# Kernel tuning notes

Measured on AMD Instinct MI355X. Metric: run time of the kernel, lower is better.

The kernel has to match this reference:

```python
import jax, jax.numpy as jnp
import numpy as np

N, K, B, D, T = 30000, 32, 8, 256, 10
NC = T + 1            # int_small_classes
LB_COL, UB_COL = 21, 22
INF = 1e18


def _ln(x, g, b, eps=1e-5):
    m = jnp.mean(x, axis=-1, keepdims=True)
    v = jnp.mean((x - m) ** 2, axis=-1, keepdims=True)
    return (x - m) * jax.lax.rsqrt(v + eps) * g + b


def _head(x, ng, nb, W1, b1, W2, b2, Wh, bh):
    # LayerNorm -> Linear -> GELU -> Linear -> GELU -> residual -> head (dropout off: eval)
    h = _ln(x, ng, nb)
    h = jax.nn.gelu(h @ W1.T + b1, approximate=False)
    h = jax.nn.gelu(h @ W2.T + b2, approximate=False)
    return (x + h) @ Wh.T + bh


def setup_inputs():
    key = jax.random.key(0)
    ks = jax.random.split(key, 32)
    s = 0.05
    inp = {}
    inp['evolved_tokens'] = jax.random.normal(ks[0], (B * K, D), jnp.float32)
    inp['var_batch'] = jnp.sort(jax.random.randint(ks[1], (N,), 0, B))
    aw = jax.random.uniform(ks[2], (N, K), jnp.float32)
    inp['attn_weights'] = aw / aw.sum(-1, keepdims=True)
    inp['var_types'] = jax.random.randint(ks[3], (N,), 0, 3)
    inp['z_var_0'] = jax.random.normal(ks[4], (N, D), jnp.float32)
    vf = 0.1 * jax.random.normal(ks[5], (N, 23), jnp.float32)
    lb = jnp.floor(jax.random.uniform(ks[6], (N,), minval=-5.0, maxval=0.0))
    ub = lb + jnp.floor(jax.random.uniform(ks[7], (N,), minval=0.0, maxval=30.0))
    ub = jnp.where(jax.random.uniform(ks[8], (N,)) < 0.1, 1e19, ub)
    inp['variable_features'] = vf.at[:, LB_COL].set(lb).at[:, UB_COL].set(ub)
    # deslice proj + fusion norm
    inp['Wp'] = s * jax.random.normal(ks[9], (D, D), jnp.float32)
    inp['bp'] = jnp.zeros((D,), jnp.float32)
    inp['fn_g'] = jnp.ones((D,), jnp.float32)
    inp['fn_b'] = jnp.zeros((D,), jnp.float32)
    # three decoder heads
    i = 10
    for name, out in (('bin', 1), ('ints', NC), ('intl', 1)):
        inp[name + '_ng'] = jnp.ones((D,), jnp.float32)
        inp[name + '_nb'] = jnp.zeros((D,), jnp.float32)
        inp[name + '_W1'] = s * jax.random.normal(ks[i], (D, D), jnp.float32)
        inp[name + '_b1'] = jnp.zeros((D,), jnp.float32)
        inp[name + '_W2'] = s * jax.random.normal(ks[i + 1], (D, D), jnp.float32)
        inp[name + '_b2'] = jnp.zeros((D,), jnp.float32)
        inp[name + '_Wh'] = s * jax.random.normal(ks[i + 2], (out, D), jnp.float32)
        inp[name + '_bh'] = (jnp.full((out,), -0.5, jnp.float32) if name == 'bin'
                             else jnp.zeros((out,), jnp.float32))
        i += 3
    return inp


def reference(evolved_tokens, var_batch, attn_weights, var_types, z_var_0,
              variable_features, Wp, bp, fn_g, fn_b,
              bin_ng, bin_nb, bin_W1, bin_b1, bin_W2, bin_b2, bin_Wh, bin_bh,
              ints_ng, ints_nb, ints_W1, ints_b1, ints_W2, ints_b2, ints_Wh, ints_bh,
              intl_ng, intl_nb, intl_W1, intl_b1, intl_W2, intl_b2, intl_Wh, intl_bh):
    # 1. deslice: attn_weights @ projected evolved tokens of the variable's graph
    proj = evolved_tokens @ Wp.T + bp          # [B*K, D]
    tok3 = proj.reshape(B, K, D)
    z_des = jnp.einsum('nk,nkd->nd', attn_weights, tok3[var_batch])  # [N, D]
    # 2. residual fusion + LayerNorm
    z_out = _ln(z_des + z_var_0, fn_g, fn_b)
    # 3. routing (extract_int_routing)
    lb = variable_features[:, LB_COL]
    ub = variable_features[:, UB_COL]
    is_int = var_types == 2
    finite = (jnp.abs(lb) < INF) & (jnp.abs(ub) < INF)
    mask_int_small = is_int & finite & ((ub - lb) <= T)
    mask_int_large = is_int & ~mask_int_small
    mask_bin = var_types == 1
    offsets = jnp.floor(lb)                                   # [N]
    ranges = jnp.clip(jnp.ceil(ub) - offsets + 1.0, 1.0, NC).astype(jnp.int32)  # [N]
    # 4. decode. Heads are evaluated densely on all N rows; the original's
    #    gather->MLP->scatter equals row-selection of these dense outputs.
    prob_bin = jax.nn.sigmoid(_head(z_out, bin_ng, bin_nb, bin_W1, bin_b1,
                                    bin_W2, bin_b2, bin_Wh, bin_bh))   # [N, 1]
    logits = _head(z_out, ints_ng, ints_nb, ints_W1, ints_b1,
                   ints_W2, ints_b2, ints_Wh, ints_bh)                 # [N, NC]
    valid = jnp.arange(NC)[None, :] < ranges[:, None]
    logits = jnp.where(valid, logits, -1e9)  # dynamic logit masking of invalid classes
    pred_large = _head(z_out, intl_ng, intl_nb, intl_W1, intl_b1,
                       intl_W2, intl_b2, intl_Wh, intl_bh)             # [N, 1]
    return (z_out, prob_bin, logits, pred_large,
            mask_bin, mask_int_small, mask_int_large, offsets, ranges)
```

## Files before the change

### kernel.cpp

```cpp
#include <hip/hip_runtime.h>
#include <math.h>

#define NV   30000
#define DD   256
#define KK   32
#define NCLS 11
#define NT   469

#define OZ  0
#define OPB 7680000
#define OLG 7710000
#define OPL 8040000
#define OMB 8070000
#define OMS 8100000
#define OML 8130000
#define OOF 8160000
#define ORG 8190000

typedef __bf16 bf16x8 __attribute__((ext_vector_type(8)));
typedef float  f32x4  __attribute__((ext_vector_type(4)));

__device__ __forceinline__ unsigned short f2b(float f) {
    unsigned u = __float_as_uint(f);
    u += 0x7fffu + ((u >> 16) & 1u);
    return (unsigned short)(u >> 16);
}

__device__ __forceinline__ float gelu_f(float x) {
    float x2 = x * x;
    float m = x * __builtin_fmaf(-0.0713548163f, x2, -1.5957691216f);
    float e = __expf(m);
    return x * __builtin_amdgcn_rcpf(1.0f + e);
}

__device__ __forceinline__ int swz(int row) { return (row + (row >> 3)) & 7; }
__device__ __forceinline__ int lidx(int row, int col) {
    return row * 256 + ((((col) >> 3) ^ swz(row)) << 3) + (col & 7);
}

struct WP {
    const float *W1, *ng, *nb, *b1, *W2, *Wh;
    unsigned short *W1e, *W2b, *Whb;
    float *b1e, *swh;
    int nc;
};

__global__ void k_prep(const float* __restrict__ et, const float* __restrict__ Wp,
                       const float* __restrict__ bp, unsigned short* __restrict__ projb,
                       WP wa, WP wb, WP wc) {
    __shared__ float es[DD];
    __shared__ float red[4], red2[4];
    if (blockIdx.y == 0) {
        int r = blockIdx.x, c = threadIdx.x;
        es[c] = et[r * DD + c];
        __syncthreads();
        const float4* w4 = (const float4*)(Wp + c * DD);
        float acc = bp[c];
#pragma unroll 16
        for (int d = 0; d < DD / 4; ++d) {
            float4 w = w4[d];
            acc += es[4 * d] * w.x + es[4 * d + 1] * w.y + es[4 * d + 2] * w.z + es[4 * d + 3] * w.w;
        }
        projb[r * DD + c] = f2b(acc);
        return;
    }
    WP wp = (blockIdx.y == 1) ? wa : ((blockIdx.y == 2) ? wb : wc);
    int j = blockIdx.x, d = threadIdx.x;
    float v1 = wp.W1[j * DD + d];
    wp.W1e[j * DD + d] = f2b(v1 * wp.ng[d]);
    wp.W2b[j * DD + d] = f2b(wp.W2[j * DD + d]);
    float p2 = 0.f;
    if (j < 16) {
        p2 = (j < wp.nc) ? wp.Wh[j * DD + d] : 0.f;
        wp.Whb[j * DD + d] = f2b(p2);
    }
    float p = v1 * wp.nb[d];
#pragma unroll
    for (int m = 1; m < 64; m <<= 1) { p += __shfl_xor(p, m); p2 += __shfl_xor(p2, m); }
    if ((d & 63) == 0) { red[d >> 6] = p; red2[d >> 6] = p2; }
    __syncthreads();
    if (d == 0) {
        wp.b1e[j] = wp.b1[j] + red[0] + red[1] + red[2] + red[3];
        if (j < 16) wp.swh[j] = red2[0] + red2[1] + red2[2] + red2[3];
    }
}

__global__ __launch_bounds__(256)
void k_zout(const unsigned short* __restrict__ projb, const int* __restrict__ vb,
            const float* __restrict__ aw, const float* __restrict__ z0,
            const float* __restrict__ g, const float* __restrict__ b,
            const float* __restrict__ vf, const int* __restrict__ vt,
            float* __restrict__ out, unsigned short* __restrict__ zhat,
            float2* __restrict__ zstat) {
    int wv = threadIdx.x >> 6, lane = threadIdx.x & 63;
    int n = blockIdx.x * 4 + wv;
    if (n >= NV) return;
    int bidx = vb[n];
    float awv = aw[n * KK + (lane & 31)];
    const ushort4* pr = (const ushort4*)(projb + (size_t)bidx * KK * DD);
    float4 acc = ((const float4*)(z0 + (size_t)n * DD))[lane];
#pragma unroll 8
    for (int k = 0; k < KK; ++k) {
        float a = __shfl(awv, k);
        ushort4 pu = pr[k * 64 + lane];
        acc.x += a * __uint_as_float((unsigned)pu.x << 16);
        acc.y += a * __uint_as_float((unsigned)pu.y << 16);
        acc.z += a * __uint_as_float((unsigned)pu.z << 16);
        acc.w += a * __uint_as_float((unsigned)pu.w << 16);
    }
    float s = acc.x + acc.y + acc.z + acc.w;
    float q = acc.x * acc.x + acc.y * acc.y + acc.z * acc.z + acc.w * acc.w;
#pragma unroll
    for (int m = 1; m < 64; m <<= 1) { s += __shfl_xor(s, m); q += __shfl_xor(q, m); }
    float mean = s * (1.f / DD);
    float var  = q * (1.f / DD) - mean * mean;
    float rs   = rsqrtf(var + 1e-5f);
    float4 g4 = ((const float4*)g)[lane], b4 = ((const float4*)b)[lane];
    float4 z;
    z.x = (acc.x - mean) * rs * g4.x + b4.x;
    z.y = (acc.y - mean) * rs * g4.y + b4.y;
    z.z = (acc.z - mean) * rs * g4.z + b4.z;
    z.w = (acc.w - mean) * rs * g4.w + b4.w;
    ((float4*)(out + OZ + (size_t)n * DD))[lane] = z;
    float s2 = z.x + z.y + z.z + z.w;
    float q2 = z.x * z.x + z.y * z.y + z.z * z.z + z.w * z.w;
#pragma unroll
    for (int m = 1; m < 64; m <<= 1) { s2 += __shfl_xor(s2, m); q2 += __shfl_xor(q2, m); }
    float m2 = s2 * (1.f / DD);
    float v2 = q2 * (1.f / DD) - m2 * m2;
    float r2 = rsqrtf(v2 + 1e-5f);
    ushort4 zh;
    zh.x = f2b((z.x - m2) * r2); zh.y = f2b((z.y - m2) * r2);
    zh.z = f2b((z.z - m2) * r2); zh.w = f2b((z.w - m2) * r2);
    int rl = n & 63;
    int c = lane >> 1;
    int pc = (c & ~7) | ((c & 7) ^ swz(rl));
    *(ushort4*)(zhat + (size_t)(n & ~63) * 256 + rl * 256 + pc * 8 + (lane & 1) * 4) = zh;
    if (lane == 0) {
        zstat[n] = make_float2((v2 + 1e-5f) * r2, m2);
        float lb = vf[n * 23 + 21], ub = vf[n * 23 + 22];
        int t = vt[n];
        bool is_int = (t == 2);
        bool finite = (fabsf(lb) < 1e18f) && (fabsf(ub) < 1e18f);
        bool small_ = is_int && finite && (ub - lb <= 10.0f);
        float off = floorf(lb);
        float rngf = ceilf(ub) - off + 1.0f;
        rngf = fminf(fmaxf(rngf, 1.0f), (float)NCLS);
        out[OMB + n] = (t == 1) ? 1.0f : 0.0f;
        out[OMS + n] = small_ ? 1.0f : 0.0f;
        out[OML + n] = (is_int && !small_) ? 1.0f : 0.0f;
        out[OOF + n] = off;
        out[ORG + n] = (float)((int)rngf);
    }
}

struct HeadP {
    const unsigned short *W1e, *W2b, *Whb;
    const float *b1e, *b2, *bh, *swh;
    int nc;
};

__global__ __launch_bounds__(256, 4)
void k_heads(const unsigned short* __restrict__ zhat, const float2* __restrict__ zstat,
             const float* __restrict__ ranges,
             HeadP h0, HeadP h1p, HeadP h2p,
             float* __restrict__ opb, float* __restrict__ olg, float* __restrict__ opl) {
    __shared__ unsigned short hl[64 * 256];
    __shared__ float b1s[DD], b2s[DD];
    __shared__ float rs2s[64], m2s[64];
    __shared__ float swhs[16], bhs[16];

    int head = blockIdx.x / NT;
    int tile = blockIdx.x % NT;
    HeadP hp = (head == 0) ? h0 : ((head == 1) ? h1p : h2p);
    int nc = hp.nc;
    int n0 = tile * 64;
    int tid = threadIdx.x;

    {
        const uint4* src = (const uint4*)(zhat + (size_t)n0 * 256);
        uint4* dst = (uint4*)hl;
#pragma unroll
        for (int j = 0; j < 8; ++j) dst[tid + j * 256] = src[tid + j * 256];
    }
    b1s[tid] = hp.b1e[tid];
    b2s[tid] = hp.b2[tid];
    if (tid < 64) {
        int n = n0 + tid;
        float2 st = (n < NV) ? zstat[n] : make_float2(0.f, 0.f);
        rs2s[tid] = st.x; m2s[tid] = st.y;
    } else if (tid < 80) {
        swhs[tid - 64] = hp.swh[tid - 64];
    } else if (tid < 96) {
        int o = tid - 80;
        bhs[o] = (o < nc) ? hp.bh[o] : 0.f;
    }

    int lane = tid & 63, wv = tid >> 6;
    int l15 = lane & 15, lq = lane >> 4;
    int nb0 = wv * 64;

    f32x4 acc[4][4];
#pragma unroll
    for (int mt = 0; mt < 4; ++mt)
#pragma unroll
        for (int nt = 0; nt < 4; ++nt) acc[mt][nt] = f32x4{0.f, 0.f, 0.f, 0.f};

    __syncthreads();

    {
        const unsigned short* Bb = hp.W1e + (size_t)(nb0 + l15) * DD + lq * 8;
        bf16x8 b[2][4], a[4];
#pragma unroll
        for (int nt = 0; nt < 4; ++nt) b[0][nt] = *(const bf16x8*)(Bb + nt * 16 * DD);
#pragma unroll
        for (int ks = 0; ks < 8; ++ks) {
            int cur = ks & 1;
            if (ks < 7) {
#pragma unroll
                for (int nt = 0; nt < 4; ++nt)
                    b[cur ^ 1][nt] = *(const bf16x8*)(Bb + nt * 16 * DD + (ks + 1) * 32);
            }
            int ck = ks * 4 + lq;
#pragma unroll
            for (int mt = 0; mt < 4; ++mt) {
                int row = mt * 16 + l15;
                int ph = (ck & ~7) | ((ck & 7) ^ swz(row));
                a[mt] = *(const bf16x8*)(hl + row * 256 + ph * 8);
            }
#pragma unroll
            for (int nt = 0; nt < 4; ++nt)
#pragma unroll
                for (int mt = 0; mt < 4; ++mt)
                    acc[mt][nt] = __builtin_amdgcn_mfma_f32_16x16x32_bf16(a[mt], b[cur][nt], acc[mt][nt], 0, 0, 0);
        }
    }
    __syncthreads();

#pragma unroll
    for (int nt = 0; nt < 4; ++nt) {
        int col = nb0 + nt * 16 + l15;
        float bias = b1s[col];
#pragma unroll
        for (int mt = 0; mt < 4; ++mt)
#pragma unroll
            for (int r = 0; r < 4; ++r) {
                int row = mt * 16 + lq * 4 + r;
                hl[lidx(row, col)] = f2b(gelu_f(acc[mt][nt][r] + bias));
            }
    }
    __syncthreads();

#pragma unroll
    for (int mt = 0; mt < 4; ++mt)
#pragma unroll
        for (int nt = 0; nt < 4; ++nt) acc[mt][nt] = f32x4{0.f, 0.f, 0.f, 0.f};
    {
        const unsigned short* Bb = hp.W2b + (size_t)(nb0 + l15) * DD + lq * 8;
        bf16x8 b[2][4], a[4];
#pragma unroll
        for (int nt = 0; nt < 4; ++nt) b[0][nt] = *(const bf16x8*)(Bb + nt * 16 * DD);
#pragma unroll
        for (int ks = 0; ks < 8; ++ks) {
            int cur = ks & 1;
            if (ks < 7) {
#pragma unroll
                for (int nt = 0; nt < 4; ++nt)
                    b[cur ^ 1][nt] = *(const bf16x8*)(Bb + nt * 16 * DD + (ks + 1) * 32);
            }
            int ck = ks * 4 + lq;
#pragma unroll
            for (int mt = 0; mt < 4; ++mt) {
                int row = mt * 16 + l15;
                int ph = (ck & ~7) | ((ck & 7) ^ swz(row));
                a[mt] = *(const bf16x8*)(hl + row * 256 + ph * 8);
            }
#pragma unroll
            for (int nt = 0; nt < 4; ++nt)
#pragma unroll
                for (int mt = 0; mt < 4; ++mt)
                    acc[mt][nt] = __builtin_amdgcn_mfma_f32_16x16x32_bf16(a[mt], b[cur][nt], acc[mt][nt], 0, 0, 0);
        }
    }

#pragma unroll
    for (int nt = 0; nt < 4; ++nt) {
        float bias = b2s[nb0 + nt * 16 + l15];
#pragma unroll
        for (int mt = 0; mt < 4; ++mt)
#pragma unroll
            for (int r = 0; r < 4; ++r)
                acc[mt][nt][r] = gelu_f(acc[mt][nt][r] + bias);
    }
    __syncthreads();

#pragma unroll
    for (int nt = 0; nt < 4; ++nt) {
        int col = nb0 + nt * 16 + l15;
#pragma unroll
        for (int mt = 0; mt < 4; ++mt)
#pragma unroll
            for (int r = 0; r < 4; ++r) {
                int row = mt * 16 + lq * 4 + r;
                hl[lidx(row, col)] = f2b(acc[mt][nt][r]);
            }
    }

    f32x4 accP[4], accZ[4];
#pragma unroll
    for (int mt = 0; mt < 4; ++mt) { accP[mt] = f32x4{0.f, 0.f, 0.f, 0.f}; accZ[mt] = f32x4{0.f, 0.f, 0.f, 0.f}; }
    {
        const unsigned short* Wb = hp.Whb + (size_t)l15 * DD + nb0 + lq * 8;
        const unsigned short* zt = zhat + (size_t)n0 * 256;
#pragma unroll
        for (int ks = 0; ks < 2; ++ks) {
            bf16x8 bP = *(const bf16x8*)(Wb + ks * 32);
            int ck = (nb0 >> 3) + ks * 4 + lq;
#pragma unroll
            for (int mt = 0; mt < 4; ++mt) {
                int row = mt * 16 + l15;
                int ph = (ck & ~7) | ((ck & 7) ^ swz(row));
                bf16x8 aP = *(const bf16x8*)(hl + row * 256 + ph * 8);
                bf16x8 aZ = *(const bf16x8*)(zt + row * 256 + ph * 8);
                accP[mt] = __builtin_amdgcn_mfma_f32_16x16x32_bf16(aP, bP, accP[mt], 0, 0, 0);
                accZ[mt] = __builtin_amdgcn_mfma_f32_16x16x32_bf16(aZ, bP, accZ[mt], 0, 0, 0);
            }
        }
    }
#pragma unroll
    for (int mt = 0; mt < 4; ++mt) {
        int rb = mt * 16 + lq * 4;
#pragma unroll
        for (int r = 0; r < 4; ++r) {
            float pv = accP[mt][r] + rs2s[rb + r] * accZ[mt][r];
            float* pp = (float*)(hl + (rb + r) * 256 + nb0);
            pp[l15] = pv;
        }
    }
    __syncthreads();

    for (int idx = tid; idx < 64 * nc; idx += 256) {
        int row, o;
        if (nc == 1) { row = idx; o = 0; }
        else { row = idx / NCLS; o = idx - row * NCLS; }
        int n = n0 + row;
        if (n < NV) {
            float val = bhs[o] + m2s[row] * swhs[o];
#pragma unroll
            for (int w2 = 0; w2 < 4; ++w2)
                val += ((const float*)(hl + row * 256 + w2 * 64))[o];
            if (head == 0)      opb[n] = __builtin_amdgcn_rcpf(1.f + __expf(-val));
            else if (head == 2) opl[n] = val;
            else {
                int rng = (int)ranges[n];
                olg[n * NCLS + o] = (o < rng) ? val : -1e9f;
            }
        }
    }
}

extern "C" void kernel_launch(void* const* d_in, const int* in_sizes, int n_in,
                              void* d_out, int out_size, void* d_ws, size_t ws_size,
                              hipStream_t stream) {
    const float* et = (const float*)d_in[0];
    const int*   vb = (const int*)d_in[1];
    const float* aw = (const float*)d_in[2];
    const int*   vt = (const int*)d_in[3];
    const float* z0 = (const float*)d_in[4];
    const float* vf = (const float*)d_in[5];
    const float* Wp = (const float*)d_in[6];
    const float* bp = (const float*)d_in[7];
    const float* fg = (const float*)d_in[8];
    const float* fb = (const float*)d_in[9];
    float* out = (float*)d_out;

    char* ws = (char*)d_ws;
    unsigned short* projb = (unsigned short*)ws;
    float* b1e           = (float*)(ws + 131072);
    unsigned short* W1e  = (unsigned short*)(ws + 134144);
    unsigned short* W2b  = (unsigned short*)(ws + 527360);
    unsigned short* Whb  = (unsigned short*)(ws + 920576);
    float* swh           = (float*)(ws + 945152);
    float2* zstat        = (float2*)(ws + 945408);
    unsigned short* zhat = (unsigned short*)(ws + 1185536);

    WP wps[3];
    for (int h = 0; h < 3; ++h) {
        wps[h].W1 = (const float*)d_in[12 + 8 * h];
        wps[h].ng = (const float*)d_in[10 + 8 * h];
        wps[h].nb = (const float*)d_in[11 + 8 * h];
        wps[h].b1 = (const float*)d_in[13 + 8 * h];
        wps[h].W2 = (const float*)d_in[14 + 8 * h];
        wps[h].Wh = (const float*)d_in[16 + 8 * h];
        wps[h].W1e = W1e + h * 65536;
        wps[h].W2b = W2b + h * 65536;
        wps[h].Whb = Whb + h * 4096;
        wps[h].b1e = b1e + h * 256;
        wps[h].swh = swh + h * 16;
        wps[h].nc  = (h == 1) ? NCLS : 1;
    }
    k_prep<<<dim3(256, 4), 256, 0, stream>>>(et, Wp, bp, projb, wps[0], wps[1], wps[2]);

    k_zout<<<7500, 256, 0, stream>>>(projb, vb, aw, z0, fg, fb, vf, vt, out, zhat, zstat);

    HeadP hps[3];
    for (int h = 0; h < 3; ++h) {
        hps[h].W1e = W1e + h * 65536;
        hps[h].W2b = W2b + h * 65536;
        hps[h].Whb = Whb + h * 4096;
        hps[h].b1e = b1e + h * 256;
        hps[h].b2  = (const float*)d_in[15 + 8 * h];
        hps[h].bh  = (const float*)d_in[17 + 8 * h];
        hps[h].swh = swh + h * 16;
        hps[h].nc  = (h == 1) ? NCLS : 1;
    }
    k_heads<<<3 * NT, 256, 0, stream>>>(zhat, zstat, out + ORG,
                                        hps[0], hps[1], hps[2],
                                        out + OPB, out + OLG, out + OPL);
}
```

Measured before the change: 279.3 us.

## Widen head kernel to 8 waves, process two rows per wave in zout

The head-MLP kernel now runs 512 threads, so each of 8 waves computes a 32-column slice instead of 64. That halves per-wave accumulators and adds parallelism per tile, and a barrier is added before the head partial sums are written into shared memory. The z_out kernel now handles two variables per wave, interleaving their gather loads to expose more memory-level parallelism. The mask, offset and range computation moves out of z_out into an extra block row of the prep kernel. The risks are more barrier cost and smaller MFMA tiles per wave in the head kernel.

```diff
diff --git a/kernel.cpp b/kernel.cpp
--- a/kernel.cpp
+++ b/kernel.cpp
@@ -47,6 +47,8 @@
 
 __global__ void k_prep(const float* __restrict__ et, const float* __restrict__ Wp,
                        const float* __restrict__ bp, unsigned short* __restrict__ projb,
+                       const float* __restrict__ vf, const int* __restrict__ vt,
+                       float* __restrict__ out,
                        WP wa, WP wb, WP wc) {
     __shared__ float es[DD];
     __shared__ float red[4], red2[4];
@@ -64,6 +66,25 @@
         projb[r * DD + c] = f2b(acc);
         return;
     }
+    if (blockIdx.y == 4) {
+        int n = blockIdx.x * 256 + threadIdx.x;
+        if (n < NV) {
+            float lb = vf[n * 23 + 21], ub = vf[n * 23 + 22];
+            int t = vt[n];
+            bool is_int = (t == 2);
+            bool finite = (fabsf(lb) < 1e18f) && (fabsf(ub) < 1e18f);
+            bool small_ = is_int && finite && (ub - lb <= 10.0f);
+            float off = floorf(lb);
+            float rngf = ceilf(ub) - off + 1.0f;
+            rngf = fminf(fmaxf(rngf, 1.0f), (float)NCLS);
+            out[OMB + n] = (t == 1) ? 1.0f : 0.0f;
+            out[OMS + n] = small_ ? 1.0f : 0.0f;
+            out[OML + n] = (is_int && !small_) ? 1.0f : 0.0f;
+            out[OOF + n] = off;
+            out[ORG + n] = (float)((int)rngf);
+        }
+        return;
+    }
     WP wp = (blockIdx.y == 1) ? wa : ((blockIdx.y == 2) ? wb : wc);
     int j = blockIdx.x, d = threadIdx.x;
     float v1 = wp.W1[j * DD + d];
@@ -89,68 +110,75 @@
 void k_zout(const unsigned short* __restrict__ projb, const int* __restrict__ vb,
             const float* __restrict__ aw, const float* __restrict__ z0,
             const float* __restrict__ g, const float* __restrict__ b,
-            const float* __restrict__ vf, const int* __restrict__ vt,
             float* __restrict__ out, unsigned short* __restrict__ zhat,
             float2* __restrict__ zstat) {
     int wv = threadIdx.x >> 6, lane = threadIdx.x & 63;
-    int n = blockIdx.x * 4 + wv;
-    if (n >= NV) return;
-    int bidx = vb[n];
-    float awv = aw[n * KK + (lane & 31)];
-    const ushort4* pr = (const ushort4*)(projb + (size_t)bidx * KK * DD);
-    float4 acc = ((const float4*)(z0 + (size_t)n * DD))[lane];
-#pragma unroll 8
+    int n0r = blockIdx.x * 8 + wv * 2;
+    if (n0r >= NV) return;
+    bool ok1 = (n0r + 1) < NV;
+    int b0 = vb[n0r];
+    int b1i = ok1 ? vb[n0r + 1] : b0;
+    float aw0 = aw[(size_t)n0r * KK + (lane & 31)];
+    float aw1 = ok1 ? aw[(size_t)(n0r + 1) * KK + (lane & 31)] : 0.f;
+    const ushort4* pr0 = (const ushort4*)(projb + (size_t)b0 * KK * DD);
+    const ushort4* pr1 = (const ushort4*)(projb + (size_t)b1i * KK * DD);
+    float4 acc0 = ((const float4*)(z0 + (size_t)n0r * DD))[lane];
+    float4 acc1 = ok1 ? ((const float4*)(z0 + (size_t)(n0r + 1) * DD))[lane]
+                      : make_float4(0.f, 0.f, 0.f, 0.f);
+#pragma unroll 4
     for (int k = 0; k < KK; ++k) {
-        float a = __shfl(awv, k);
-        ushort4 pu = pr[k * 64 + lane];
-        acc.x += a * __uint_as_float((unsigned)pu.x << 16);
-        acc.y += a * __uint_as_float((unsigned)pu.y << 16);
-        acc.z += a * __uint_as_float((unsigned)pu.z << 16);
-        acc.w += a * __uint_as_float((unsigned)pu.w << 16);
-    }
-    float s = acc.x + acc.y + acc.z + acc.w;
-    float q = acc.x * acc.x + acc.y * acc.y + acc.z * acc.z + acc.w * acc.w;
-#pragma unroll
-    for (int m = 1; m < 64; m <<= 1) { s += __shfl_xor(s, m); q += __shfl_xor(q, m); }
-    float mean = s * (1.f / DD);
-    float var  = q * (1.f / DD) - mean * mean;
-    float rs   = rsqrtf(var + 1e-5f);
+        float a0 = __shfl(aw0, k), a1 = __shfl(aw1, k);
+        ushort4 p0 = pr0[k * 64 + lane];
+        ushort4 p1 = pr1[k * 64 + lane];
+        acc0.x += a0 * __uint_as_float((unsigned)p0.x << 16);
+        acc0.y += a0 * __uint_as_float((unsigned)p0.y << 16);
+        acc0.z += a0 * __uint_as_float((unsigned)p0.z << 16);
+        acc0.w += a0 * __uint_as_float((unsigned)p0.w << 16);
+        acc1.x += a1 * __uint_as_float((unsigned)p1.x << 16);
+        acc1.y += a1 * __uint_as_float((unsigned)p1.y << 16);
+        acc1.z += a1 * __uint_as_float((unsigned)p1.z << 16);
+        acc1.w += a1 * __uint_as_float((unsigned)p1.w << 16);
+    }
+    float s0 = acc0.x + acc0.y + acc0.z + acc0.w;
+    float q0 = acc0.x * acc0.x + acc0.y * acc0.y + acc0.z * acc0.z + acc0.w * acc0.w;
+    float s1 = acc1.x + acc1.y + acc1.z + acc1.w;
+    float q1 = acc1.x * acc1.x + acc1.y * acc1.y + acc1.z * acc1.z + acc1.w * acc1.w;
+#pragma unroll
+    for (int m = 1; m < 64; m <<= 1) {
+        s0 += __shfl_xor(s0, m); q0 += __shfl_xor(q0, m);
+        s1 += __shfl_xor(s1, m); q1 += __shfl_xor(q1, m);
+    }
     float4 g4 = ((const float4*)g)[lane], b4 = ((const float4*)b)[lane];
-    float4 z;
-    z.x = (acc.x - mean) * rs * g4.x + b4.x;
-    z.y = (acc.y - mean) * rs * g4.y + b4.y;
-    z.z = (acc.z - mean) * rs * g4.z + b4.z;
-    z.w = (acc.w - mean) * rs * g4.w + b4.w;
-    ((float4*)(out + OZ + (size_t)n * DD))[lane] = z;
-    float s2 = z.x + z.y + z.z + z.w;
-    float q2 = z.x * z.x + z.y * z.y + z.z * z.z + z.w * z.w;
-#pragma unroll
-    for (int m = 1; m < 64; m <<= 1) { s2 += __shfl_xor(s2, m); q2 += __shfl_xor(q2, m); }
-    float m2 = s2 * (1.f / DD);
-    float v2 = q2 * (1.f / DD) - m2 * m2;
-    float r2 = rsqrtf(v2 + 1e-5f);
-    ushort4 zh;
-    zh.x = f2b((z.x - m2) * r2); zh.y = f2b((z.y - m2) * r2);
-    zh.z = f2b((z.z - m2) * r2); zh.w = f2b((z.w - m2) * r2);
-    int rl = n & 63;
-    int c = lane >> 1;
-    int pc = (c & ~7) | ((c & 7) ^ swz(rl));
-    *(ushort4*)(zhat + (size_t)(n & ~63) * 256 + rl * 256 + pc * 8 + (lane & 1) * 4) = zh;
-    if (lane == 0) {
-        zstat[n] = make_float2((v2 + 1e-5f) * r2, m2);
-        float lb = vf[n * 23 + 21], ub = vf[n * 23 + 22];
-        int t = vt[n];
-        bool is_int = (t == 2);
-        bool finite = (fabsf(lb) < 1e18f) && (fabsf(ub) < 1e18f);
-        bool small_ = is_int && finite && (ub - lb <= 10.0f);
-        float off = floorf(lb);
-        float rngf = ceilf(ub) - off + 1.0f;
-        rngf = fminf(fmaxf(rngf, 1.0f), (float)NCLS);
-        out[OMB + n] = (t == 1) ? 1.0f : 0.0f;
-        out[OMS + n] = small_ ? 1.0f : 0.0f;
-        out[OML + n] = (is_int && !small_) ? 1.0f : 0.0f;
-        out[OOF + n] = off;
-        out[ORG + n] = (float)((int)rngf);
+#pragma unroll
+    for (int rr = 0; rr < 2; ++rr) {
+        int n = n0r + rr;
+        if (rr && !ok1) break;
+        float4 acc = rr ? acc1 : acc0;
+        float s = rr ? s1 : s0, q = rr ? q1 : q0;
+        float mean = s * (1.f / DD);
+        float var  = q * (1.f / DD) - mean * mean;
+        float rs   = rsqrtf(var + 1e-5f);
+        float4 z;
+        z.x = (acc.x - mean) * rs * g4.x + b4.x;
+        z.y = (acc.y - mean) * rs * g4.y + b4.y;
+        z.z = (acc.z - mean) * rs * g4.z + b4.z;
+        z.w = (acc.w - mean) * rs * g4.w + b4.w;
+        ((float4*)(out + OZ + (size_t)n * DD))[lane] = z;
+        float s2 = z.x + z.y + z.z + z.w;
+        float q2 = z.x * z.x + z.y * z.y + z.z * z.z + z.w * z.w;
+#pragma unroll
+        for (int m = 1; m < 64; m <<= 1) { s2 += __shfl_xor(s2, m); q2 += __shfl_xor(q2, m); }
+        float m2 = s2 * (1.f / DD);
+        float v2 = q2 * (1.f / DD) - m2 * m2;
+        float r2 = rsqrtf(v2 + 1e-5f);
+        ushort4 zh;
+        zh.x = f2b((z.x - m2) * r2); zh.y = f2b((z.y - m2) * r2);
+        zh.z = f2b((z.z - m2) * r2); zh.w = f2b((z.w - m2) * r2);
+        int rl = n & 63;
+        int c = lane >> 1;
+        int pc = (c & ~7) | ((c & 7) ^ swz(rl));
+        *(ushort4*)(zhat + (size_t)(n & ~63) * 256 + rl * 256 + pc * 8 + (lane & 1) * 4) = zh;
+        if (lane == 0) zstat[n] = make_float2((v2 + 1e-5f) * r2, m2);
     }
 }
 
@@ -160,7 +188,7 @@
     int nc;
 };
 
-__global__ __launch_bounds__(256, 4)
+__global__ __launch_bounds__(512, 4)
 void k_heads(const unsigned short* __restrict__ zhat, const float2* __restrict__ zstat,
              const float* __restrict__ ranges,
              HeadP h0, HeadP h1p, HeadP h2p,
@@ -181,10 +209,10 @@
         const uint4* src = (const uint4*)(zhat + (size_t)n0 * 256);
         uint4* dst = (uint4*)hl;
 #pragma unroll
-        for (int j = 0; j < 8; ++j) dst[tid + j * 256] = src[tid + j * 256];
-    }
-    b1s[tid] = hp.b1e[tid];
-    b2s[tid] = hp.b2[tid];
+        for (int j = 0; j < 4; ++j) dst[tid + j * 512] = src[tid + j * 512];
+    }
+    if (tid < 256) b1s[tid] = hp.b1e[tid];
+    else           b2s[tid - 256] = hp.b2[tid - 256];
     if (tid < 64) {
         int n = n0 + tid;
         float2 st = (n < NV) ? zstat[n] : make_float2(0.f, 0.f);
@@ -198,27 +226,27 @@
 
     int lane = tid & 63, wv = tid >> 6;
     int l15 = lane & 15, lq = lane >> 4;
-    int nb0 = wv * 64;
-
-    f32x4 acc[4][4];
+    int nb0 = wv * 32;
+
+    f32x4 acc[4][2];
 #pragma unroll
     for (int mt = 0; mt < 4; ++mt)
 #pragma unroll
-        for (int nt = 0; nt < 4; ++nt) acc[mt][nt] = f32x4{0.f, 0.f, 0.f, 0.f};
+        for (int nt = 0; nt < 2; ++nt) acc[mt][nt] = f32x4{0.f, 0.f, 0.f, 0.f};
 
     __syncthreads();
 
     {
         const unsigned short* Bb = hp.W1e + (size_t)(nb0 + l15) * DD + lq * 8;
-        bf16x8 b[2][4], a[4];
-#pragma unroll
-        for (int nt = 0; nt < 4; ++nt) b[0][nt] = *(const bf16x8*)(Bb + nt * 16 * DD);
+        bf16x8 b[2][2], a[4];
+#pragma unroll
+        for (int nt = 0; nt < 2; ++nt) b[0][nt] = *(const bf16x8*)(Bb + nt * 16 * DD);
 #pragma unroll
         for (int ks = 0; ks < 8; ++ks) {
             int cur = ks & 1;
             if (ks < 7) {
 #pragma unroll
-                for (int nt = 0; nt < 4; ++nt)
+                for (int nt = 0; nt < 2; ++nt)
                     b[cur ^ 1][nt] = *(const bf16x8*)(Bb + nt * 16 * DD + (ks + 1) * 32);
             }
             int ck = ks * 4 + lq;
@@ -229,7 +257,7 @@
                 a[mt] = *(const bf16x8*)(hl + row * 256 + ph * 8);
             }
 #pragma unroll
-            for (int nt = 0; nt < 4; ++nt)
+            for (int nt = 0; nt < 2; ++nt)
 #pragma unroll
                 for (int mt = 0; mt < 4; ++mt)
                     acc[mt][nt] = __builtin_amdgcn_mfma_f32_16x16x32_bf16(a[mt], b[cur][nt], acc[mt][nt], 0, 0, 0);
@@ -238,7 +266,7 @@
     __syncthreads();
 
 #pragma unroll
-    for (int nt = 0; nt < 4; ++nt) {
+    for (int nt = 0; nt < 2; ++nt) {
         int col = nb0 + nt * 16 + l15;
         float bias = b1s[col];
 #pragma unroll
@@ -254,18 +282,18 @@
 #pragma unroll
     for (int mt = 0; mt < 4; ++mt)
 #pragma unroll
-        for (int nt = 0; nt < 4; ++nt) acc[mt][nt] = f32x4{0.f, 0.f, 0.f, 0.f};
+        for (int nt = 0; nt < 2; ++nt) acc[mt][nt] = f32x4{0.f, 0.f, 0.f, 0.f};
     {
         const unsigned short* Bb = hp.W2b + (size_t)(nb0 + l15) * DD + lq * 8;
-        bf16x8 b[2][4], a[4];
-#pragma unroll
-        for (int nt = 0; nt < 4; ++nt) b[0][nt] = *(const bf16x8*)(Bb + nt * 16 * DD);
+        bf16x8 b[2][2], a[4];
+#pragma unroll
+        for (int nt = 0; nt < 2; ++nt) b[0][nt] = *(const bf16x8*)(Bb + nt * 16 * DD);
 #pragma unroll
         for (int ks = 0; ks < 8; ++ks) {
             int cur = ks & 1;
             if (ks < 7) {
 #pragma unroll
-                for (int nt = 0; nt < 4; ++nt)
+                for (int nt = 0; nt < 2; ++nt)
                     b[cur ^ 1][nt] = *(const bf16x8*)(Bb + nt * 16 * DD + (ks + 1) * 32);
             }
             int ck = ks * 4 + lq;
@@ -276,7 +304,7 @@
                 a[mt] = *(const bf16x8*)(hl + row * 256 + ph * 8);
             }
 #pragma unroll
-            for (int nt = 0; nt < 4; ++nt)
+            for (int nt = 0; nt < 2; ++nt)
 #pragma unroll
                 for (int mt = 0; mt < 4; ++mt)
                     acc[mt][nt] = __builtin_amdgcn_mfma_f32_16x16x32_bf16(a[mt], b[cur][nt], acc[mt][nt], 0, 0, 0);
@@ -284,7 +312,7 @@
     }
 
 #pragma unroll
-    for (int nt = 0; nt < 4; ++nt) {
+    for (int nt = 0; nt < 2; ++nt) {
         float bias = b2s[nb0 + nt * 16 + l15];
 #pragma unroll
         for (int mt = 0; mt < 4; ++mt)
@@ -295,7 +323,7 @@
     __syncthreads();
 
 #pragma unroll
-    for (int nt = 0; nt < 4; ++nt) {
+    for (int nt = 0; nt < 2; ++nt) {
         int col = nb0 + nt * 16 + l15;
 #pragma unroll
         for (int mt = 0; mt < 4; ++mt)
@@ -312,21 +340,20 @@
     {
         const unsigned short* Wb = hp.Whb + (size_t)l15 * DD + nb0 + lq * 8;
         const unsigned short* zt = zhat + (size_t)n0 * 256;
-#pragma unroll
-        for (int ks = 0; ks < 2; ++ks) {
-            bf16x8 bP = *(const bf16x8*)(Wb + ks * 32);
-            int ck = (nb0 >> 3) + ks * 4 + lq;
-#pragma unroll
-            for (int mt = 0; mt < 4; ++mt) {
-                int row = mt * 16 + l15;
-                int ph = (ck & ~7) | ((ck & 7) ^ swz(row));
-                bf16x8 aP = *(const bf16x8*)(hl + row * 256 + ph * 8);
-                bf16x8 aZ = *(const bf16x8*)(zt + row * 256 + ph * 8);
-                accP[mt] = __builtin_amdgcn_mfma_f32_16x16x32_bf16(aP, bP, accP[mt], 0, 0, 0);
-                accZ[mt] = __builtin_amdgcn_mfma_f32_16x16x32_bf16(aZ, bP, accZ[mt], 0, 0, 0);
-            }
-        }
-    }
+        bf16x8 bP = *(const bf16x8*)(Wb);
+        int ck = (nb0 >> 3) + lq;
+#pragma unroll
+        for (int mt = 0; mt < 4; ++mt) {
+            int row = mt * 16 + l15;
+            int ph = (ck & ~7) | ((ck & 7) ^ swz(row));
+            bf16x8 aP = *(const bf16x8*)(hl + row * 256 + ph * 8);
+            bf16x8 aZ = *(const bf16x8*)(zt + row * 256 + ph * 8);
+            accP[mt] = __builtin_amdgcn_mfma_f32_16x16x32_bf16(aP, bP, accP[mt], 0, 0, 0);
+            accZ[mt] = __builtin_amdgcn_mfma_f32_16x16x32_bf16(aZ, bP, accZ[mt], 0, 0, 0);
+        }
+    }
+    __syncthreads();
+
 #pragma unroll
     for (int mt = 0; mt < 4; ++mt) {
         int rb = mt * 16 + lq * 4;
@@ -339,7 +366,7 @@
     }
     __syncthreads();
 
-    for (int idx = tid; idx < 64 * nc; idx += 256) {
+    for (int idx = tid; idx < 64 * nc; idx += 512) {
         int row, o;
         if (nc == 1) { row = idx; o = 0; }
         else { row = idx / NCLS; o = idx - row * NCLS; }
@@ -347,8 +374,8 @@
         if (n < NV) {
             float val = bhs[o] + m2s[row] * swhs[o];
 #pragma unroll
-            for (int w2 = 0; w2 < 4; ++w2)
-                val += ((const float*)(hl + row * 256 + w2 * 64))[o];
+            for (int w2 = 0; w2 < 8; ++w2)
+                val += ((const float*)(hl + row * 256 + w2 * 32))[o];
             if (head == 0)      opb[n] = __builtin_amdgcn_rcpf(1.f + __expf(-val));
             else if (head == 2) opl[n] = val;
             else {
@@ -399,9 +426,10 @@
         wps[h].swh = swh + h * 16;
         wps[h].nc  = (h == 1) ? NCLS : 1;
     }
-    k_prep<<<dim3(256, 4), 256, 0, stream>>>(et, Wp, bp, projb, wps[0], wps[1], wps[2]);
-
-    k_zout<<<7500, 256, 0, stream>>>(projb, vb, aw, z0, fg, fb, vf, vt, out, zhat, zstat);
+    k_prep<<<dim3(256, 5), 256, 0, stream>>>(et, Wp, bp, projb, vf, vt, out,
+                                             wps[0], wps[1], wps[2]);
+
+    k_zout<<<3750, 256, 0, stream>>>(projb, vb, aw, z0, fg, fb, out, zhat, zstat);
 
     HeadP hps[3];
     for (int h = 0; h < 3; ++h) {
@@ -414,7 +442,7 @@
         hps[h].swh = swh + h * 16;
         hps[h].nc  = (h == 1) ? NCLS : 1;
     }
-    k_heads<<<3 * NT, 256, 0, stream>>>(zhat, zstat, out + ORG,
+    k_heads<<<3 * NT, 512, 0, stream>>>(zhat, zstat, out + ORG,
                                         hps[0], hps[1], hps[2],
                                         out + OPB, out + OLG, out + OPL);
 }
```

Result: faster. 250.2 us (-10.4%).
